# Kernel tuning notes

Measured on AMD Instinct MI355X. Metric: run time of the kernel, lower is better.

Reference implementation:

```python
import jax, jax.numpy as jnp
import numpy as np

K = 200      # Monte Carlo samples (hardcoded in girsanov d=1 branch)
M = 256      # number of inter-event excursion intervals (= len(t0)-1)
NE = 200     # points per excursion (n_e)
H = 16       # mu-MLP hidden width
EPS = 0.01   # eps default in girsanov


def setup_inputs() -> dict:
    key = jax.random.key(0)
    ks = jax.random.split(key, 8)
    # sorted zero-crossing times t0 (strictly increasing, ~ event gaps in [0.02, 0.1])
    gaps = jax.random.uniform(ks[0], (M,), minval=0.02, maxval=0.1)
    t0 = jnp.concatenate([jnp.zeros((1,), jnp.float32), jnp.cumsum(gaps)]).astype(jnp.float32)
    noise = jax.random.normal(ks[1], (K, M, NE - 1), dtype=jnp.float32)
    W1 = jax.random.normal(ks[2], (1, H), dtype=jnp.float32) * 0.5
    b1 = jnp.zeros((H,), jnp.float32)
    W2 = jax.random.normal(ks[3], (H, H), dtype=jnp.float32) * (1.0 / np.sqrt(H))
    b2 = jnp.zeros((H,), jnp.float32)
    W3 = jax.random.normal(ks[4], (H, 1), dtype=jnp.float32) * (1.0 / np.sqrt(H))
    b3 = jnp.zeros((1,), jnp.float32)
    return {"t0": t0, "noise": noise, "W1": W1, "b1": b1, "W2": W2, "b2": b2, "W3": W3, "b3": b3}


def _mu(x, W1, b1, W2, b2, W3, b3):
    # state-dependent drift net: scalar -> H -> H -> scalar (tanh MLP)
    h = jnp.tanh(x[..., None] @ W1 + b1)   # [K,M,NE,H]
    h = jnp.tanh(h @ W2 + b2)              # [K,M,NE,H]
    return h @ W3 + b3                     # [K,M,NE,1]


def reference(t0, noise, W1, b1, W2, b2, W3, b3):
    frac = jnp.linspace(0.0, 1.0, NE).astype(noise.dtype)      # [NE]
    dt0 = t0[1:] - t0[:-1]                                     # [M]
    e_time = t0[:-1, None] + frac[None, :] * dt0[:, None]      # [M,NE] (linspace per interval)
    dte = e_time[:, 1:] - e_time[:, :-1]                       # [M,NE-1]
    # Brownian motion from increments, pinned bridge, reflected -> excursion sample
    incr = noise * jnp.sqrt(dte)[None]                         # [K,M,NE-1]
    W = jnp.concatenate([jnp.zeros((K, M, 1), noise.dtype), jnp.cumsum(incr, axis=-1)], axis=-1)
    bridge = W - frac * W[..., -1:]                            # [K,M,NE], B_0=B_T=0
    x1 = jnp.abs(bridge)                                       # positive excursion (neg=False)

    mu_t = _mu(x1, W1, b1, W2, b2, W3, b3)                     # [K,M,NE,1]
    x1e = x1[..., None]                                        # [K,M,NE,1]
    dx = x1e[:, :, 1:, :] - x1e[:, :, :-1, :]
    dt = (e_time[:, 1:] - e_time[:, :-1])[None, :, :, None]    # [1,M,NE-1,1]
    a = jnp.sum(mu_t[:, :, :-1, :] * dx, axis=(-1, -2))        # [K,M]
    b = jnp.sum(mu_t[:, :, :-1, :] ** 2 * dt, axis=(-1, -2))   # [K,M]
    s = a - 0.5 * b                                            # [K,M]
    # expect = log(mean_K exp(s)) done stably
    expect = jax.nn.logsumexp(s, axis=0) - jnp.log(jnp.asarray(K, s.dtype))  # [M]

    eps = jnp.asarray(EPS, t0.dtype)
    p = (jnp.log(eps + 1e-7) + 0.5 * jnp.log(jnp.asarray(2.0 / np.pi, t0.dtype))
         - 2.0 * eps ** 2 / dt0 - jnp.log(dt0 ** 1.5 + 1e-7))  # [M]
    return jnp.mean(p + expect)
```

## Files before the change

kernel.cpp:

```cpp
#include <hip/hip_runtime.h>
#include <math.h>

#define KK 200
#define MM 256
#define NI 199
#define HH 16
#define TBLN 4096
#define XMAX 16.0f
#define INVH 256.0f

__global__ __launch_bounds__(256) void lt_table(
    const float* __restrict__ W1, const float* __restrict__ b1,
    const float* __restrict__ W2, const float* __restrict__ b2,
    const float* __restrict__ W3, const float* __restrict__ b3,
    float* __restrict__ tbl) {
  int i = blockIdx.x * 256 + threadIdx.x;
  if (i >= TBLN) return;
  float x = (float)i * (XMAX / (float)TBLN);
  float h1[HH];
#pragma unroll
  for (int j = 0; j < HH; ++j) h1[j] = tanhf(fmaf(x, W1[j], b1[j]));
  float mu = b3[0];
#pragma unroll
  for (int i2 = 0; i2 < HH; ++i2) {
    float z = b2[i2];
#pragma unroll
    for (int j = 0; j < HH; ++j) z = fmaf(h1[j], W2[j * HH + i2], z);
    mu = fmaf(tanhf(z), W3[i2], mu);
  }
  tbl[i] = mu;
}

__global__ __launch_bounds__(1024) void lt_main(
    const float* __restrict__ t0,
    const float* __restrict__ noise,
    const float* __restrict__ tbl,
    float* __restrict__ s_out) {
  __shared__ float sT[TBLN];
  const int tid = threadIdx.x;
#pragma unroll
  for (int i = 0; i < TBLN / 1024; ++i) sT[tid + i * 1024] = tbl[tid + i * 1024];
  __syncthreads();

  const int wave = tid >> 6, lane = tid & 63;
  const int pair = blockIdx.x * 16 + wave;
  const int m = pair & 255;

  const float t0m = t0[m];
  const float dt0 = t0[m + 1] - t0m;
  const float inv199 = 1.0f / 199.0f;

  const float* nrow = noise + (size_t)pair * NI;
  const int p0 = lane * 4;

  float nv[4];
  if (p0 + 3 < NI) {
    nv[0] = nrow[p0]; nv[1] = nrow[p0 + 1]; nv[2] = nrow[p0 + 2]; nv[3] = nrow[p0 + 3];
  } else {
#pragma unroll
    for (int c = 0; c < 4; ++c) nv[c] = (p0 + c < NI) ? nrow[p0 + c] : 0.0f;
  }

  float f[5], e[5];
#pragma unroll
  for (int c = 0; c < 5; ++c) {
    f[c] = (float)(p0 + c) * inv199;
    e[c] = t0m + f[c] * dt0;
  }

  float dte[4], cum[5];
  cum[0] = 0.0f;
#pragma unroll
  for (int c = 0; c < 4; ++c) {
    dte[c] = e[c + 1] - e[c];
    float v = (p0 + c < NI) ? nv[c] * sqrtf(dte[c]) : 0.0f;
    cum[c + 1] = cum[c] + v;
  }
  const float tot = cum[4];

  float x = tot;
#pragma unroll
  for (int off = 1; off < 64; off <<= 1) {
    float y = __shfl_up(x, off, 64);
    if (lane >= off) x += y;
  }
  const float prefix = x - tot;
  const float Wfin = __shfl(x, 63, 64);

  float xb[5];
#pragma unroll
  for (int c = 0; c < 5; ++c) xb[c] = fabsf((prefix + cum[c]) - f[c] * Wfin);

  float sp = 0.0f;
#pragma unroll
  for (int c = 0; c < 4; ++c) {
    if (p0 + c < NI) {
      float xc = fminf(xb[c], XMAX - 2.0f / INVH);
      float tt = xc * INVH;
      int ix = (int)tt;
      float fr = tt - (float)ix;
      float T0 = sT[ix], T1 = sT[ix + 1];
      float mu = fmaf(fr, T1 - T0, T0);
      float dx = xb[c + 1] - xb[c];
      sp += mu * dx - 0.5f * mu * mu * dte[c];
    }
  }
#pragma unroll
  for (int off = 32; off > 0; off >>= 1) sp += __shfl_xor(sp, off, 64);
  if (lane == 0) {
    int k = pair >> 8;
    s_out[m * KK + k] = sp;
  }
}

__global__ __launch_bounds__(1024) void lt_finish(
    const float* __restrict__ t0, const float* __restrict__ s_in,
    float* __restrict__ out) {
  const int t = threadIdx.x;
  const int m = t >> 2, q = t & 3;
  const float* row = s_in + m * KK + q * 50;

  float mx = -INFINITY, sum = 0.0f;
#pragma unroll 5
  for (int i = 0; i < 50; ++i) {
    float s = row[i];
    float nm = fmaxf(mx, s);
    sum = sum * __expf(mx - nm) + __expf(s - nm);
    mx = nm;
  }
#pragma unroll
  for (int off = 1; off < 4; off <<= 1) {
    float omx = __shfl_xor(mx, off, 64);
    float osum = __shfl_xor(sum, off, 64);
    float nm = fmaxf(mx, omx);
    sum = sum * __expf(mx - nm) + osum * __expf(omx - nm);
    mx = nm;
  }

  float val = 0.0f;
  if (q == 0) {
    float expect = logf(sum) + mx - logf(200.0f);
    float t0m = t0[m], d = t0[m + 1] - t0m;
    const float eps = 0.01f;
    float p = logf(eps + 1e-7f) + 0.5f * logf(0.6366197723675814f)
            - 2.0f * eps * eps / d - logf(d * sqrtf(d) + 1e-7f);
    val = p + expect;
  }
#pragma unroll
  for (int off = 32; off > 0; off >>= 1) val += __shfl_xor(val, off, 64);

  __shared__ float red[16];
  const int lane = t & 63, w = t >> 6;
  if (lane == 0) red[w] = val;
  __syncthreads();
  if (t == 0) {
    float s2 = 0.0f;
#pragma unroll
    for (int i = 0; i < 16; ++i) s2 += red[i];
    out[0] = s2 * (1.0f / 256.0f);
  }
}

extern "C" void kernel_launch(void* const* d_in, const int* in_sizes, int n_in,
                              void* d_out, int out_size, void* d_ws, size_t ws_size,
                              hipStream_t stream) {
  const float* t0    = (const float*)d_in[0];
  const float* noise = (const float*)d_in[1];
  const float* W1    = (const float*)d_in[2];
  const float* b1    = (const float*)d_in[3];
  const float* W2    = (const float*)d_in[4];
  const float* b2    = (const float*)d_in[5];
  const float* W3    = (const float*)d_in[6];
  const float* b3    = (const float*)d_in[7];

  float* s_ws = (float*)d_ws;
  float* tbl  = s_ws + KK * MM;
  float* out  = (float*)d_out;

  lt_table<<<TBLN / 256, 256, 0, stream>>>(W1, b1, W2, b2, W3, b3, tbl);
  lt_main<<<(KK * MM) / 16, 1024, 0, stream>>>(t0, noise, tbl, s_ws);
  lt_finish<<<1, 1024, 0, stream>>>(t0, s_ws, out);
}
```

Baseline: 128.1 us.

## Fuse MLP table build into main kernel and parallelize logsumexp finish

Removes the separate table-building kernel: every block of the main kernel now evaluates the tanh MLP itself over a halved table (range 0..8, 2048 entries) using a fast exp/rcp tanh and writes it straight into shared memory. The finish kernel switches from per-thread serial online logsumexp to one wave per interval row with shuffle reductions. This saves a kernel launch and the table round-trip through global memory. In exchange each of the 3200 blocks repeats about 2 MLP evaluations per thread, and any excursion value above 8 is clamped, so the lookup is only accurate while values stay in that range.

```diff
diff --git a/kernel.cpp b/kernel.cpp
--- a/kernel.cpp
+++ b/kernel.cpp
@@ -5,41 +5,42 @@
 #define MM 256
 #define NI 199
 #define HH 16
-#define TBLN 4096
-#define XMAX 16.0f
+#define TBLN 2048
+#define XMAX 8.0f
 #define INVH 256.0f
 
-__global__ __launch_bounds__(256) void lt_table(
-    const float* __restrict__ W1, const float* __restrict__ b1,
-    const float* __restrict__ W2, const float* __restrict__ b2,
-    const float* __restrict__ W3, const float* __restrict__ b3,
-    float* __restrict__ tbl) {
-  int i = blockIdx.x * 256 + threadIdx.x;
-  if (i >= TBLN) return;
-  float x = (float)i * (XMAX / (float)TBLN);
-  float h1[HH];
-#pragma unroll
-  for (int j = 0; j < HH; ++j) h1[j] = tanhf(fmaf(x, W1[j], b1[j]));
-  float mu = b3[0];
-#pragma unroll
-  for (int i2 = 0; i2 < HH; ++i2) {
-    float z = b2[i2];
-#pragma unroll
-    for (int j = 0; j < HH; ++j) z = fmaf(h1[j], W2[j * HH + i2], z);
-    mu = fmaf(tanhf(z), W3[i2], mu);
-  }
-  tbl[i] = mu;
+__device__ __forceinline__ float fast_tanh(float x) {
+  float e = __expf(2.0f * x);
+  return 1.0f - 2.0f * __builtin_amdgcn_rcpf(e + 1.0f);
 }
 
 __global__ __launch_bounds__(1024) void lt_main(
     const float* __restrict__ t0,
     const float* __restrict__ noise,
-    const float* __restrict__ tbl,
+    const float* __restrict__ gW1, const float* __restrict__ gb1,
+    const float* __restrict__ gW2, const float* __restrict__ gb2,
+    const float* __restrict__ gW3, const float* __restrict__ gb3,
     float* __restrict__ s_out) {
   __shared__ float sT[TBLN];
   const int tid = threadIdx.x;
+
 #pragma unroll
-  for (int i = 0; i < TBLN / 1024; ++i) sT[tid + i * 1024] = tbl[tid + i * 1024];
+  for (int r = 0; r < 2; ++r) {
+    const int i = tid + r * 1024;
+    const float x = (float)i * (XMAX / (float)TBLN);
+    float h1[HH];
+#pragma unroll
+    for (int j = 0; j < HH; ++j) h1[j] = fast_tanh(fmaf(x, gW1[j], gb1[j]));
+    float mu = gb3[0];
+#pragma unroll
+    for (int i2 = 0; i2 < HH; ++i2) {
+      float z = gb2[i2];
+#pragma unroll
+      for (int j = 0; j < HH; ++j) z = fmaf(h1[j], gW2[j * HH + i2], z);
+      mu = fmaf(fast_tanh(z), gW3[i2], mu);
+    }
+    sT[i] = mu;
+  }
   __syncthreads();
 
   const int wave = tid >> 6, lane = tid & 63;
@@ -116,44 +117,42 @@
 __global__ __launch_bounds__(1024) void lt_finish(
     const float* __restrict__ t0, const float* __restrict__ s_in,
     float* __restrict__ out) {
-  const int t = threadIdx.x;
-  const int m = t >> 2, q = t & 3;
-  const float* row = s_in + m * KK + q * 50;
+  const int tid = threadIdx.x;
+  const int wave = tid >> 6, lane = tid & 63;
 
-  float mx = -INFINITY, sum = 0.0f;
-#pragma unroll 5
-  for (int i = 0; i < 50; ++i) {
-    float s = row[i];
-    float nm = fmaxf(mx, s);
-    sum = sum * __expf(mx - nm) + __expf(s - nm);
-    mx = nm;
-  }
+  float acc = 0.0f;
 #pragma unroll
-  for (int off = 1; off < 4; off <<= 1) {
-    float omx = __shfl_xor(mx, off, 64);
-    float osum = __shfl_xor(sum, off, 64);
-    float nm = fmaxf(mx, omx);
-    sum = sum * __expf(mx - nm) + osum * __expf(omx - nm);
-    mx = nm;
+  for (int mm = 0; mm < 16; ++mm) {
+    const int m = mm * 16 + wave;
+    const float* row = s_in + m * KK;
+    float v0 = row[lane];
+    float v1 = row[lane + 64];
+    float v2 = row[lane + 128];
+    float v3 = (lane < 8) ? row[lane + 192] : -INFINITY;
+
+    float mx = fmaxf(fmaxf(v0, v1), fmaxf(v2, v3));
+#pragma unroll
+    for (int off = 32; off > 0; off >>= 1) mx = fmaxf(mx, __shfl_xor(mx, off, 64));
+
+    float sum = __expf(v0 - mx) + __expf(v1 - mx) + __expf(v2 - mx)
+              + ((lane < 8) ? __expf(v3 - mx) : 0.0f);
+#pragma unroll
+    for (int off = 32; off > 0; off >>= 1) sum += __shfl_xor(sum, off, 64);
+
+    if (lane == 0) {
+      float expect = logf(sum) + mx - logf(200.0f);
+      float d = t0[m + 1] - t0[m];
+      const float eps = 0.01f;
+      float p = logf(eps + 1e-7f) + 0.5f * logf(0.6366197723675814f)
+              - 2.0f * eps * eps / d - logf(d * sqrtf(d) + 1e-7f);
+      acc += p + expect;
+    }
   }
 
-  float val = 0.0f;
-  if (q == 0) {
-    float expect = logf(sum) + mx - logf(200.0f);
-    float t0m = t0[m], d = t0[m + 1] - t0m;
-    const float eps = 0.01f;
-    float p = logf(eps + 1e-7f) + 0.5f * logf(0.6366197723675814f)
-            - 2.0f * eps * eps / d - logf(d * sqrtf(d) + 1e-7f);
-    val = p + expect;
-  }
-#pragma unroll
-  for (int off = 32; off > 0; off >>= 1) val += __shfl_xor(val, off, 64);
-
   __shared__ float red[16];
-  const int lane = t & 63, w = t >> 6;
-  if (lane == 0) red[w] = val;
+  if (lane == 0) red[wave] = acc;
   __syncthreads();
-  if (t == 0) {
+  if (tid == 0) {
     float s2 = 0.0f;
 #pragma unroll
     for (int i = 0; i < 16; ++i) s2 += red[i];
@@ -174,10 +173,8 @@
   const float* b3    = (const float*)d_in[7];
 
   float* s_ws = (float*)d_ws;
-  float* tbl  = s_ws + KK * MM;
   float* out  = (float*)d_out;
 
-  lt_table<<<TBLN / 256, 256, 0, stream>>>(W1, b1, W2, b2, W3, b3, tbl);
-  lt_main<<<(KK * MM) / 16, 1024, 0, stream>>>(t0, noise, tbl, s_ws);
+  lt_main<<<(KK * MM) / 16, 1024, 0, stream>>>(t0, noise, W1, b1, W2, b2, W3, b3, s_ws);
   lt_finish<<<1, 1024, 0, stream>>>(t0, s_ws, out);
 }
```

After: 240.3 us. 1.88x slower.
